# Kernel tuning notes

Hardware: AMD Instinct MI355X
Metric: run time of the kernel (lower is better)

## Reference

```python
import jax, jax.numpy as jnp
import numpy as np

ALPHA = 1.5
BETA = 0.5
AVG_RATIO = 1.0
SUM_TIMESTEPS = 28000
RANK = 8
K_TOP = RANK * RANK  # k = weight_1_a.shape[1] * weight_2_a.shape[1]


def setup_inputs() -> dict:
    key = jax.random.key(0)
    ks = jax.random.split(key, 5)
    B, S, D_IN, D_OUT = 2, 4096, 4096, 4096
    return {
        "hidden_states": jax.random.normal(ks[0], (B, S, D_IN), dtype=jnp.float32),
        "weight_1_a": jax.random.normal(ks[1], (D_OUT, RANK), dtype=jnp.float32) * 0.02,
        "weight_1_b": jax.random.normal(ks[2], (RANK, D_IN), dtype=jnp.float32) * 0.02,
        "weight_2_a": jax.random.normal(ks[3], (D_OUT, RANK), dtype=jnp.float32) * 0.02,
        "weight_2_b": jax.random.normal(ks[4], (RANK, D_IN), dtype=jnp.float32) * 0.02,
        "timestep": 1,
    }


def reference(hidden_states, weight_1_a, weight_1_b, weight_2_a, weight_2_b, timestep):
    # Low-rank expansions: [out, rank] @ [rank, in] -> [out, in]
    matrix1 = weight_1_a @ weight_1_b
    matrix2 = weight_2_a @ weight_2_b
    top_k_sum1 = jax.lax.top_k(jnp.abs(matrix1).ravel(), K_TOP)[0].sum()
    top_k_sum2 = jax.lax.top_k(jnp.abs(matrix2).ravel(), K_TOP)[0].sum()
    time_ratio = timestep % SUM_TIMESTEPS
    scale = (ALPHA * time_ratio / SUM_TIMESTEPS + BETA) % ALPHA  # pattern 's*'
    temp_ratio = (top_k_sum1 / AVG_RATIO) / (top_k_sum2 * scale)
    weight = jnp.where(temp_ratio > 1.0, matrix1, matrix2)  # [out, in]
    # F.linear: x @ W^T
    return jnp.einsum("bsi,oi->bso", hidden_states, weight)
```

## Files before the change

kernel.cpp:

```cpp
#include <hip/hip_runtime.h>
#include <stdint.h>

#define D 4096
#define RANK 8
#define ALPHA 1.5f
#define BETA 0.5f
#define SUM_TIMESTEPS 28000
#define K_TOP 64
#define NBINS 1024

typedef float f32x4 __attribute__((ext_vector_type(4)));

#define WS_GCNT_OFF 256
#define WS_GSUM_OFF (256 + 2 * NBINS * 4)
#define WS_BMAX_OFF (WS_GSUM_OFF + 2 * NBINS * 8)

#define FIX_NUM 2.74877906944e11f
#define FIX_INV 3.637978807091713e-12

__device__ __forceinline__ float dot4v(f32x4 a, f32x4 b) {
    return fmaf(a.x, b.x, fmaf(a.y, b.y, fmaf(a.z, b.z, a.w * b.w)));
}

__global__ __launch_bounds__(256) void k_pass_max(
    const float* __restrict__ wa1, const float* __restrict__ wb1,
    const float* __restrict__ wa2, const float* __restrict__ wb2,
    unsigned* __restrict__ gz, unsigned* __restrict__ bmax) {
    const int tid = threadIdx.x;
    const int mat = blockIdx.y;
    const int bid = blockIdx.x;
    if (mat == 0 && tid < 24) gz[bid * 24 + tid] = 0u;

    const float* __restrict__ wa = mat ? wa2 : wa1;
    const float* __restrict__ wb = mat ? wb2 : wb1;
    const int i0 = (bid & 3) * 1024 + tid * 4;
    const int obase = (bid >> 2) * 64;

    f32x4 wbv[RANK];
#pragma unroll
    for (int r = 0; r < RANK; ++r)
        wbv[r] = *(const f32x4*)(wb + r * D + i0);

    float vmax = 0.f;
#pragma unroll 4
    for (int oo = 0; oo < 64; ++oo) {
        const float* __restrict__ war = wa + (size_t)(obase + oo) * RANK;
        f32x4 s = {0.f, 0.f, 0.f, 0.f};
#pragma unroll
        for (int r = 0; r < RANK; ++r) {
            const float a = war[r];
            s.x = fmaf(a, wbv[r].x, s.x);
            s.y = fmaf(a, wbv[r].y, s.y);
            s.z = fmaf(a, wbv[r].z, s.z);
            s.w = fmaf(a, wbv[r].w, s.w);
        }
        vmax = fmaxf(vmax, fmaxf(fmaxf(fabsf(s.x), fabsf(s.y)),
                                 fmaxf(fabsf(s.z), fabsf(s.w))));
    }
    for (int off = 32; off; off >>= 1)
        vmax = fmaxf(vmax, __shfl_xor(vmax, off, 64));
    __shared__ float smax[4];
    const int wave = tid >> 6, lane = tid & 63;
    if (lane == 0) smax[wave] = vmax;
    __syncthreads();
    if (tid == 0) {
        float m = fmaxf(fmaxf(smax[0], smax[1]), fmaxf(smax[2], smax[3]));
        bmax[mat * 256 + bid] = __float_as_uint(m);
    }
}

__device__ __forceinline__ float block_max256(const unsigned* __restrict__ bmax,
                                              int mat, int tid, float* redm) {
    const int wave = tid >> 6, lane = tid & 63;
    float m = 0.f;
    if (tid < 256) m = __uint_as_float(bmax[mat * 256 + tid]);
    for (int off = 32; off; off >>= 1)
        m = fmaxf(m, __shfl_xor(m, off, 64));
    if (tid < 256 && lane == 0) redm[wave] = m;
    __syncthreads();
    return fmaxf(fmaxf(redm[0], redm[1]), fmaxf(redm[2], redm[3]));
}

__global__ __launch_bounds__(256) void k_pass_hist(
    const float* __restrict__ wa1, const float* __restrict__ wb1,
    const float* __restrict__ wa2, const float* __restrict__ wb2,
    const unsigned* __restrict__ bmax,
    unsigned* __restrict__ gcnt, unsigned long long* __restrict__ gsum) {
    __shared__ unsigned lcnt[NBINS];
    __shared__ unsigned long long lsum[NBINS];
    __shared__ float redm[4];
    const int tid = threadIdx.x;
    const int mat = blockIdx.y;
    for (int b = tid; b < NBINS; b += 256) { lcnt[b] = 0u; lsum[b] = 0ull; }
    const float M = block_max256(bmax, mat, tid, redm);

    const float* __restrict__ wa = mat ? wa2 : wa1;
    const float* __restrict__ wb = mat ? wb2 : wb1;
    const float T = 0.5f * M;
    const float fix = FIX_NUM / M;
    const unsigned bitsT = __float_as_uint(T);
    const int i0 = (blockIdx.x & 3) * 1024 + tid * 4;
    const int obase = (blockIdx.x >> 2) * 64;

    f32x4 wbv[RANK];
#pragma unroll
    for (int r = 0; r < RANK; ++r)
        wbv[r] = *(const f32x4*)(wb + r * D + i0);

#pragma unroll 2
    for (int oo = 0; oo < 64; ++oo) {
        const float* __restrict__ war = wa + (size_t)(obase + oo) * RANK;
        f32x4 s = {0.f, 0.f, 0.f, 0.f};
#pragma unroll
        for (int r = 0; r < RANK; ++r) {
            const float a = war[r];
            s.x = fmaf(a, wbv[r].x, s.x);
            s.y = fmaf(a, wbv[r].y, s.y);
            s.z = fmaf(a, wbv[r].z, s.z);
            s.w = fmaf(a, wbv[r].w, s.w);
        }
        const float av[4] = {fabsf(s.x), fabsf(s.y), fabsf(s.z), fabsf(s.w)};
#pragma unroll
        for (int j = 0; j < 4; ++j) {
            if (av[j] >= T) {
                unsigned k = (__float_as_uint(av[j]) - bitsT) >> 13;
                if (k > NBINS - 1u) k = NBINS - 1u;
                atomicAdd(&lcnt[k], 1u);
                atomicAdd(&lsum[k], (unsigned long long)(av[j] * fix));
            }
        }
    }
    __syncthreads();
    unsigned* __restrict__ gc = gcnt + (size_t)mat * NBINS;
    unsigned long long* __restrict__ gs = gsum + (size_t)mat * NBINS;
    for (int b = tid; b < NBINS; b += 256) {
        unsigned c = lcnt[b];
        if (c) {
            atomicAdd(&gc[b], c);
            atomicAdd(&gs[b], lsum[b]);
        }
    }
}

__global__ __launch_bounds__(1024) void k_select(
    unsigned* __restrict__ hdr, const unsigned* __restrict__ bmax,
    const unsigned* __restrict__ gcnt, const unsigned long long* __restrict__ gsum,
    const int* __restrict__ tsp) {
    __shared__ unsigned sc[NBINS];
    __shared__ unsigned long long ss[NBINS];
    __shared__ float res[2];
    __shared__ float Ms[2];
    __shared__ float redm[4];
    __shared__ int sB;
    const int b = threadIdx.x;

    for (int mat = 0; mat < 2; ++mat) {
        float M = block_max256(bmax, mat, b, redm);
        if (b == 0) Ms[mat] = M;
        __syncthreads();
    }

    for (int mat = 0; mat < 2; ++mat) {
        if (b == 0) sB = -1;
        const unsigned c0 = gcnt[(size_t)mat * NBINS + b];
        const unsigned long long s0 = gsum[(size_t)mat * NBINS + b];
        __syncthreads();
        sc[b] = c0;
        ss[b] = s0;
        __syncthreads();
        for (int step = 1; step < NBINS; step <<= 1) {
            unsigned c2 = 0u; unsigned long long s2 = 0ull;
            if (b + step < NBINS) { c2 = sc[b + step]; s2 = ss[b + step]; }
            __syncthreads();
            sc[b] += c2;
            ss[b] += s2;
            __syncthreads();
        }
        if (sc[b] >= K_TOP && (b == NBINS - 1 || sc[b + 1] < K_TOP)) sB = b;
        __syncthreads();
        if (b == 0) {
            const double inv = (double)Ms[mat] * FIX_INV;
            float total;
            if (sB < 0) {
                total = (float)((double)ss[0] * inv);
            } else {
                const int B = sB;
                const unsigned cAbove = (B + 1 < NBINS) ? sc[B + 1] : 0u;
                const unsigned long long sAbove = (B + 1 < NBINS) ? ss[B + 1] : 0ull;
                const unsigned cb = sc[B] - cAbove;
                const unsigned long long sb = ss[B] - sAbove;
                const unsigned need = K_TOP - cAbove;
                total = (float)((double)sAbove * inv)
                      + (float)((double)sb * inv) * ((float)need / (float)cb);
            }
            res[mat] = total;
        }
        __syncthreads();
    }
    if (b == 0) {
        const int tr = (*tsp) % SUM_TIMESTEPS;
        const float scale = fmodf(ALPHA * (float)tr / (float)SUM_TIMESTEPS + BETA, ALPHA);
        const float temp_ratio = res[0] / (res[1] * scale);
        hdr[4] = (temp_ratio > 1.0f) ? 1u : 0u;
    }
}

__global__ __launch_bounds__(256) void k_fused(
    const float* __restrict__ h,
    const float* __restrict__ wa1, const float* __restrict__ wb1,
    const float* __restrict__ wa2, const float* __restrict__ wb2,
    const unsigned* __restrict__ hdr,
    float* __restrict__ out) {
    const int tid = threadIdx.x;
    const int wave = tid >> 6, lane = tid & 63;
    const unsigned flag = hdr[4];
    const float* __restrict__ wa = flag ? wa1 : wa2;
    const float* __restrict__ wb = flag ? wb1 : wb2;
    const size_t m0 = (size_t)blockIdx.x * 16;
    const int r0w = wave * 4;

    __shared__ float wbs[RANK][1024];
    __shared__ float ts[16][8];

    float acc[4][RANK];
#pragma unroll
    for (int row = 0; row < 4; ++row)
#pragma unroll
        for (int r = 0; r < RANK; ++r) acc[row][r] = 0.f;

    for (int q = 0; q < 4; ++q) {
        __syncthreads();
        {
            const f32x4* __restrict__ src = (const f32x4*)wb;
            f32x4* __restrict__ dst = (f32x4*)wbs;
#pragma unroll
            for (int t = 0; t < 8; ++t) {
                const int j = t * 256 + tid;
                const int r = j >> 8;
                const int c = j & 255;
                dst[j] = src[r * 1024 + q * 256 + c];
            }
        }
        __syncthreads();
#pragma unroll
        for (int k = 0; k < 4; ++k) {
            const int il = k * 256 + lane * 4;
            f32x4 wbv[RANK];
#pragma unroll
            for (int r = 0; r < RANK; ++r)
                wbv[r] = *(const f32x4*)&wbs[r][il];
            f32x4 hv[4];
#pragma unroll
            for (int row = 0; row < 4; ++row)
                hv[row] = *(const f32x4*)(h + (m0 + r0w + row) * D + q * 1024 + il);
#pragma unroll
            for (int row = 0; row < 4; ++row)
#pragma unroll
                for (int r = 0; r < RANK; ++r)
                    acc[row][r] = fmaf(hv[row].x, wbv[r].x,
                                  fmaf(hv[row].y, wbv[r].y,
                                  fmaf(hv[row].z, wbv[r].z,
                                  fmaf(hv[row].w, wbv[r].w, acc[row][r]))));
        }
    }

#pragma unroll
    for (int row = 0; row < 4; ++row)
#pragma unroll
        for (int r = 0; r < RANK; ++r)
#pragma unroll
            for (int off = 32; off; off >>= 1)
                acc[row][r] += __shfl_xor(acc[row][r], off, 64);
    if (lane == 0) {
#pragma unroll
        for (int row = 0; row < 4; ++row)
#pragma unroll
            for (int r = 0; r < RANK; ++r)
                ts[r0w + row][r] = acc[row][r];
    }
    __syncthreads();

#pragma unroll
    for (int cc = 0; cc < 4; ++cc) {
        const int o0 = wave * 1024 + cc * 256 + lane * 4;
        f32x4 A[8];
#pragma unroll
        for (int j = 0; j < 8; ++j)
            A[j] = *(const f32x4*)(wa + (size_t)o0 * RANK + j * 4);
#pragma unroll 4
        for (int row = 0; row < 16; ++row) {
            const f32x4 t03 = *(const f32x4*)&ts[row][0];
            const f32x4 t47 = *(const f32x4*)&ts[row][4];
            f32x4 ov;
            ov.x = dot4v(A[0], t03) + dot4v(A[1], t47);
            ov.y = dot4v(A[2], t03) + dot4v(A[3], t47);
            ov.z = dot4v(A[4], t03) + dot4v(A[5], t47);
            ov.w = dot4v(A[6], t03) + dot4v(A[7], t47);
            __builtin_nontemporal_store(ov, (f32x4*)(out + (m0 + row) * D + o0));
        }
    }
}

extern "C" void kernel_launch(void* const* d_in, const int* in_sizes, int n_in,
                              void* d_out, int out_size, void* d_ws, size_t ws_size,
                              hipStream_t stream) {
    const float* h   = (const float*)d_in[0];
    const float* wa1 = (const float*)d_in[1];
    const float* wb1 = (const float*)d_in[2];
    const float* wa2 = (const float*)d_in[3];
    const float* wb2 = (const float*)d_in[4];
    const int*   ts  = (const int*)d_in[5];
    float* out = (float*)d_out;

    const int rows = in_sizes[0] / D;

    unsigned* hdr  = (unsigned*)d_ws;
    unsigned* gcnt = (unsigned*)((char*)d_ws + WS_GCNT_OFF);
    unsigned long long* gsum = (unsigned long long*)((char*)d_ws + WS_GSUM_OFF);
    unsigned* bmax = (unsigned*)((char*)d_ws + WS_BMAX_OFF);

    hipLaunchKernelGGL(k_pass_max, dim3(256, 2), dim3(256), 0, stream,
                       wa1, wb1, wa2, wb2, gcnt, bmax);
    hipLaunchKernelGGL(k_pass_hist, dim3(256, 2), dim3(256), 0, stream,
                       wa1, wb1, wa2, wb2, bmax, gcnt, gsum);
    hipLaunchKernelGGL(k_select, dim3(1), dim3(1024), 0, stream,
                       hdr, bmax, gcnt, gsum, ts);
    hipLaunchKernelGGL(k_fused, dim3(rows / 16), dim3(256), 0, stream,
                       h, wa1, wb1, wa2, wb2, hdr, out);
}
```

Before: 107.4 us.

## Stage wa rows in LDS and prefetch loads ahead in main GEMM kernel

The max and histogram passes now load each block's 64x8 slice of weight_a into shared memory once, so rows come from LDS instead of scalar global loads inside the loop. In the main kernel, the hidden-state loads for a whole 1024-wide chunk are issued together with the wb staging loads before the LDS store barrier, so global latency overlaps the LDS fill. The next output chunk's weight_a columns are also prefetched while the current chunk is stored. The cost is higher register pressure (hv[4][4], An[8]), which can reduce occupancy.

Result: faster. 92.35 us (-14.0%).

```diff
diff --git a/kernel.cpp b/kernel.cpp
--- a/kernel.cpp
+++ b/kernel.cpp
@@ -36,23 +36,29 @@
     const int i0 = (bid & 3) * 1024 + tid * 4;
     const int obase = (bid >> 2) * 64;
 
+    __shared__ float was[64][8];
+    if (tid < 128)
+        ((f32x4*)was)[tid] = ((const f32x4*)(wa + (size_t)obase * RANK))[tid];
+
     f32x4 wbv[RANK];
 #pragma unroll
     for (int r = 0; r < RANK; ++r)
         wbv[r] = *(const f32x4*)(wb + r * D + i0);
+    __syncthreads();
 
     float vmax = 0.f;
 #pragma unroll 4
     for (int oo = 0; oo < 64; ++oo) {
-        const float* __restrict__ war = wa + (size_t)(obase + oo) * RANK;
+        const f32x4 w03 = *(const f32x4*)&was[oo][0];
+        const f32x4 w47 = *(const f32x4*)&was[oo][4];
         f32x4 s = {0.f, 0.f, 0.f, 0.f};
+        const float a[8] = {w03.x, w03.y, w03.z, w03.w, w47.x, w47.y, w47.z, w47.w};
 #pragma unroll
         for (int r = 0; r < RANK; ++r) {
-            const float a = war[r];
-            s.x = fmaf(a, wbv[r].x, s.x);
-            s.y = fmaf(a, wbv[r].y, s.y);
-            s.z = fmaf(a, wbv[r].z, s.z);
-            s.w = fmaf(a, wbv[r].w, s.w);
+            s.x = fmaf(a[r], wbv[r].x, s.x);
+            s.y = fmaf(a[r], wbv[r].y, s.y);
+            s.z = fmaf(a[r], wbv[r].z, s.z);
+            s.w = fmaf(a[r], wbv[r].w, s.w);
         }
         vmax = fmaxf(vmax, fmaxf(fmaxf(fabsf(s.x), fabsf(s.y)),
                                  fmaxf(fabsf(s.z), fabsf(s.w))));
@@ -88,19 +94,23 @@
     unsigned* __restrict__ gcnt, unsigned long long* __restrict__ gsum) {
     __shared__ unsigned lcnt[NBINS];
     __shared__ unsigned long long lsum[NBINS];
+    __shared__ float was[64][8];
     __shared__ float redm[4];
     const int tid = threadIdx.x;
     const int mat = blockIdx.y;
     for (int b = tid; b < NBINS; b += 256) { lcnt[b] = 0u; lsum[b] = 0ull; }
-    const float M = block_max256(bmax, mat, tid, redm);
 
     const float* __restrict__ wa = mat ? wa2 : wa1;
     const float* __restrict__ wb = mat ? wb2 : wb1;
+    const int i0 = (blockIdx.x & 3) * 1024 + tid * 4;
+    const int obase = (blockIdx.x >> 2) * 64;
+    if (tid < 128)
+        ((f32x4*)was)[tid] = ((const f32x4*)(wa + (size_t)obase * RANK))[tid];
+
+    const float M = block_max256(bmax, mat, tid, redm);
     const float T = 0.5f * M;
     const float fix = FIX_NUM / M;
     const unsigned bitsT = __float_as_uint(T);
-    const int i0 = (blockIdx.x & 3) * 1024 + tid * 4;
-    const int obase = (blockIdx.x >> 2) * 64;
 
     f32x4 wbv[RANK];
 #pragma unroll
@@ -109,15 +119,16 @@
 
 #pragma unroll 2
     for (int oo = 0; oo < 64; ++oo) {
-        const float* __restrict__ war = wa + (size_t)(obase + oo) * RANK;
+        const f32x4 w03 = *(const f32x4*)&was[oo][0];
+        const f32x4 w47 = *(const f32x4*)&was[oo][4];
         f32x4 s = {0.f, 0.f, 0.f, 0.f};
+        const float a[8] = {w03.x, w03.y, w03.z, w03.w, w47.x, w47.y, w47.z, w47.w};
 #pragma unroll
         for (int r = 0; r < RANK; ++r) {
-            const float a = war[r];
-            s.x = fmaf(a, wbv[r].x, s.x);
-            s.y = fmaf(a, wbv[r].y, s.y);
-            s.z = fmaf(a, wbv[r].z, s.z);
-            s.w = fmaf(a, wbv[r].w, s.w);
+            s.x = fmaf(a[r], wbv[r].x, s.x);
+            s.y = fmaf(a[r], wbv[r].y, s.y);
+            s.z = fmaf(a[r], wbv[r].z, s.z);
+            s.w = fmaf(a[r], wbv[r].w, s.w);
         }
         const float av[4] = {fabsf(s.x), fabsf(s.y), fabsf(s.z), fabsf(s.w)};
 #pragma unroll
@@ -228,19 +239,26 @@
 #pragma unroll
         for (int r = 0; r < RANK; ++r) acc[row][r] = 0.f;
 
+    const f32x4* __restrict__ src = (const f32x4*)wb;
+    f32x4* __restrict__ dst = (f32x4*)wbs;
+
     for (int q = 0; q < 4; ++q) {
         __syncthreads();
-        {
-            const f32x4* __restrict__ src = (const f32x4*)wb;
-            f32x4* __restrict__ dst = (f32x4*)wbs;
-#pragma unroll
-            for (int t = 0; t < 8; ++t) {
-                const int j = t * 256 + tid;
-                const int r = j >> 8;
-                const int c = j & 255;
-                dst[j] = src[r * 1024 + q * 256 + c];
-            }
-        }
+        f32x4 sreg[8];
+#pragma unroll
+        for (int t = 0; t < 8; ++t) {
+            const int j = t * 256 + tid;
+            sreg[t] = src[(j >> 8) * 1024 + q * 256 + (j & 255)];
+        }
+        f32x4 hv[4][4];
+#pragma unroll
+        for (int k = 0; k < 4; ++k)
+#pragma unroll
+            for (int row = 0; row < 4; ++row)
+                hv[k][row] = *(const f32x4*)(h + (m0 + r0w + row) * D
+                                             + q * 1024 + k * 256 + lane * 4);
+#pragma unroll
+        for (int t = 0; t < 8; ++t) dst[t * 256 + tid] = sreg[t];
         __syncthreads();
 #pragma unroll
         for (int k = 0; k < 4; ++k) {
@@ -249,18 +267,14 @@
 #pragma unroll
             for (int r = 0; r < RANK; ++r)
                 wbv[r] = *(const f32x4*)&wbs[r][il];
-            f32x4 hv[4];
 #pragma unroll
             for (int row = 0; row < 4; ++row)
-                hv[row] = *(const f32x4*)(h + (m0 + r0w + row) * D + q * 1024 + il);
-#pragma unroll
-            for (int row = 0; row < 4; ++row)
 #pragma unroll
                 for (int r = 0; r < RANK; ++r)
-                    acc[row][r] = fmaf(hv[row].x, wbv[r].x,
-                                  fmaf(hv[row].y, wbv[r].y,
-                                  fmaf(hv[row].z, wbv[r].z,
-                                  fmaf(hv[row].w, wbv[r].w, acc[row][r]))));
+                    acc[row][r] = fmaf(hv[k][row].x, wbv[r].x,
+                                  fmaf(hv[k][row].y, wbv[r].y,
+                                  fmaf(hv[k][row].z, wbv[r].z,
+                                  fmaf(hv[k][row].w, wbv[r].w, acc[row][r]))));
         }
     }
 
@@ -280,13 +294,21 @@
     }
     __syncthreads();
 
-#pragma unroll
-    for (int cc = 0; cc < 4; ++cc) {
-        const int o0 = wave * 1024 + cc * 256 + lane * 4;
-        f32x4 A[8];
+    f32x4 A[8], An[8];
+    {
+        const int o0 = wave * 1024 + lane * 4;
 #pragma unroll
         for (int j = 0; j < 8; ++j)
             A[j] = *(const f32x4*)(wa + (size_t)o0 * RANK + j * 4);
+    }
+    for (int cc = 0; cc < 4; ++cc) {
+        if (cc < 3) {
+            const int o1 = wave * 1024 + (cc + 1) * 256 + lane * 4;
+#pragma unroll
+            for (int j = 0; j < 8; ++j)
+                An[j] = *(const f32x4*)(wa + (size_t)o1 * RANK + j * 4);
+        }
+        const int o0 = wave * 1024 + cc * 256 + lane * 4;
 #pragma unroll 4
         for (int row = 0; row < 16; ++row) {
             const f32x4 t03 = *(const f32x4*)&ts[row][0];
@@ -298,6 +320,10 @@
             ov.w = dot4v(A[6], t03) + dot4v(A[7], t47);
             __builtin_nontemporal_store(ov, (f32x4*)(out + (m0 + row) * D + o0));
         }
+        if (cc < 3) {
+#pragma unroll
+            for (int j = 0; j < 8; ++j) A[j] = An[j];
+        }
     }
 }
 
```
